# Kernel tuning notes

Measured on AMD Instinct MI355X. Metric: run time of the kernel, lower is better.

Reference implementation:

```python
import jax, jax.numpy as jnp
import numpy as np
from jax import lax

B, N, M = 2, 16384, 4096
C1, C2 = 128, 256
H1, H2 = 256, 128  # mlp = [C1+C2, 256, 128]


def setup_inputs() -> dict:
    key = jax.random.key(0)
    ks = jax.random.split(key, 8)
    return {
        "unknown": jax.random.normal(ks[0], (B, N, 3), jnp.float32),
        "known": jax.random.normal(ks[1], (B, M, 3), jnp.float32),
        "unknow_feats": jax.random.normal(ks[2], (B, C1, N), jnp.float32),
        "known_feats": jax.random.normal(ks[3], (B, C2, M), jnp.float32),
        "W1": jax.random.normal(ks[4], (H1, C1 + C2), jnp.float32) * 0.05,
        "b1": jnp.zeros((H1,), jnp.float32),
        "W2": jax.random.normal(ks[5], (H2, H1), jnp.float32) * 0.05,
        "b2": jnp.zeros((H2,), jnp.float32),
    }


def reference(unknown, known, unknow_feats, known_feats, W1, b1, W2, b2):
    # Pairwise squared distances (B, n, m) via ||a||^2 + ||b||^2 - 2 a.b
    d2 = (
        jnp.sum(unknown * unknown, -1)[:, :, None]
        + jnp.sum(known * known, -1)[:, None, :]
        - 2.0 * jnp.einsum("bnd,bmd->bnm", unknown, known)
    )
    # 3 nearest neighbors
    neg_d2, idx = lax.top_k(-d2, 3)  # (B, n, 3)
    dist = jnp.sqrt(jnp.maximum(-neg_d2, 0.0))  # pointops returns sqrt distances
    dist_recip = 1.0 / (dist + 1e-8)
    weight = dist_recip / jnp.sum(dist_recip, axis=2, keepdims=True)  # (B, n, 3)
    # Gather neighbor features (B, C2, n, 3) and inverse-distance weighted sum
    gathered = jax.vmap(lambda f, i: f[:, i])(known_feats, idx)
    interpolated = jnp.sum(gathered * weight[:, None, :, :], axis=-1)  # (B, C2, n)
    new_features = jnp.concatenate([interpolated, unknow_feats], axis=1)  # (B, C1+C2, n)
    # Shared MLP (1x1 convs, bn=False -> conv bias + ReLU)
    h = jax.nn.relu(jnp.einsum("oc,bcn->bon", W1, new_features) + b1[None, :, None])
    out = jax.nn.relu(jnp.einsum("oc,bcn->bon", W2, h) + b2[None, :, None])
    return out  # (B, mlp[-1], n)
```

## Files before the change

kernel.cpp:

```cpp
#include <hip/hip_runtime.h>
#include <hip/hip_bf16.h>

#define BB 2
#define NN 16384
#define MM 4096
#define C1 128
#define C2 256
#define CIN 384
#define H1 256
#define H2 128
#define PT 32

typedef __attribute__((ext_vector_type(8))) short bf16x8;
typedef __attribute__((ext_vector_type(4))) float f32x4;
typedef __attribute__((ext_vector_type(2))) float f32x2;
typedef __attribute__((ext_vector_type(8))) float f32x8;

__device__ __forceinline__ short f32_to_bf16(float x) {
    unsigned u = __float_as_uint(x);
    u += 0x7fffu + ((u >> 16) & 1u);
    return (short)(u >> 16);
}
__device__ __forceinline__ unsigned pack_bf16x2(float a, float b) {
    __hip_bfloat162 h = __float22bfloat162_rn(make_float2(a, b));
    union { __hip_bfloat162 h; unsigned u; } cv;
    cv.h = h;
    return cv.u;
}

__global__ __launch_bounds__(256) void prep_transpose_kernel(
    const float* __restrict__ KF, float* __restrict__ KT,
    const float* __restrict__ W1, const float* __restrict__ W2,
    const float* __restrict__ known,
    short* __restrict__ W1b, short* __restrict__ W2b,
    float* __restrict__ kpk8)
{
    const int bx = blockIdx.x;
    if (bx < 2048) {
        __shared__ float tl[32][33];
        const int b  = bx >> 10;
        const int c0 = ((bx >> 7) & 7) * 32;
        const int m0 = (bx & 127) * 32;
        const int tx = threadIdx.x & 31;
        const int ty = threadIdx.x >> 5;
        #pragma unroll
        for (int r = 0; r < 4; ++r) {
            int c = ty + r * 8;
            tl[c][tx] = KF[((size_t)b * C2 + c0 + c) * MM + m0 + tx];
        }
        __syncthreads();
        #pragma unroll
        for (int r = 0; r < 4; ++r) {
            int m = ty + r * 8;
            KT[((size_t)b * MM + m0 + m) * C2 + c0 + tx] = tl[tx][m];
        }
    } else {
        int i = (bx - 2048) * 256 + threadIdx.x;
        if (i < H1 * CIN) W1b[i] = f32_to_bf16(W1[i]);
        if (i < H2 * H1)  W2b[i] = f32_to_bf16(W2[i]);
        if (i < BB * MM) {
            float x = known[3 * i + 0], y = known[3 * i + 1], z = known[3 * i + 2];
            float n = fmaf(x, x, fmaf(y, y, z * z));
            int g = i >> 1, j = i & 1;
            float* base = kpk8 + (size_t)g * 8;
            base[0 + j] = x; base[2 + j] = y; base[4 + j] = z; base[6 + j] = n;
        }
    }
}

__global__ __launch_bounds__(1024) void knn3_kernel(
    const float* __restrict__ unknown,
    const float* __restrict__ kpk8,
    int*   __restrict__ idx_out,
    float* __restrict__ w_out)
{
    __shared__ float pdv[16][64][3];
    __shared__ float vf[64];
    __shared__ float msc[64][8];
    __shared__ int   mid[64][8];
    __shared__ int   cnt[64];

    const int b    = blockIdx.y;
    const int tid  = threadIdx.x;
    const int lane = tid & 63;
    const int wv   = __builtin_amdgcn_readfirstlane(tid >> 6);
    const int n    = blockIdx.x * 64 + lane;

    if (tid < 64) cnt[tid] = 0;

    const float ux = unknown[((size_t)b * NN + n) * 3 + 0];
    const float uy = unknown[((size_t)b * NN + n) * 3 + 1];
    const float uz = unknown[((size_t)b * NN + n) * 3 + 2];
    const f32x2 ax2 = {-2.f * ux, -2.f * ux};
    const f32x2 ay2 = {-2.f * uy, -2.f * uy};
    const f32x2 az2 = {-2.f * uz, -2.f * uz};
    const float un = fmaf(ux, ux, fmaf(uy, uy, uz * uz));

    const int gbase = wv * 128;
    const float* __restrict__ kp = kpk8 + ((size_t)b * (MM / 2) + gbase) * 8;

    float v0 = 3e38f, v1 = 3e38f, v2 = 3e38f;
    #pragma unroll 4
    for (int g = 0; g < 128; ++g) {
        const f32x8 G = *(const f32x8*)(kp + (size_t)g * 8);
        const f32x2 kx = __builtin_shufflevector(G, G, 0, 1);
        const f32x2 ky = __builtin_shufflevector(G, G, 2, 3);
        const f32x2 kz = __builtin_shufflevector(G, G, 4, 5);
        const f32x2 kn = __builtin_shufflevector(G, G, 6, 7);
        const f32x2 sc2 = __builtin_elementwise_fma(ax2, kx,
                          __builtin_elementwise_fma(ay2, ky,
                          __builtin_elementwise_fma(az2, kz, kn)));
        float sa = sc2.x;
        v2 = __builtin_amdgcn_fmed3f(v1, sa, v2);
        v1 = __builtin_amdgcn_fmed3f(v0, sa, v1);
        v0 = fminf(sa, v0);
        float sb = sc2.y;
        v2 = __builtin_amdgcn_fmed3f(v1, sb, v2);
        v1 = __builtin_amdgcn_fmed3f(v0, sb, v1);
        v0 = fminf(sb, v0);
    }
    pdv[wv][lane][0] = v0; pdv[wv][lane][1] = v1; pdv[wv][lane][2] = v2;
    __syncthreads();

    if (tid < 64) {
        float r0 = 3e38f, r1 = 3e38f, r2 = 3e38f;
        #pragma unroll
        for (int ww = 0; ww < 16; ++ww) {
            #pragma unroll
            for (int k = 0; k < 3; ++k) {
                float d = pdv[ww][tid][k];
                r2 = __builtin_amdgcn_fmed3f(r1, d, r2);
                r1 = __builtin_amdgcn_fmed3f(r0, d, r1);
                r0 = fminf(d, r0);
            }
        }
        vf[tid] = r2;
    }
    __syncthreads();

    const float v2f = vf[lane];
    #pragma unroll 4
    for (int g = 0; g < 128; ++g) {
        const f32x8 G = *(const f32x8*)(kp + (size_t)g * 8);
        const f32x2 kx = __builtin_shufflevector(G, G, 0, 1);
        const f32x2 ky = __builtin_shufflevector(G, G, 2, 3);
        const f32x2 kz = __builtin_shufflevector(G, G, 4, 5);
        const f32x2 kn = __builtin_shufflevector(G, G, 6, 7);
        const f32x2 sc2 = __builtin_elementwise_fma(ax2, kx,
                          __builtin_elementwise_fma(ay2, ky,
                          __builtin_elementwise_fma(az2, kz, kn)));
        if (fminf(sc2.x, sc2.y) <= v2f) {
            if (sc2.x <= v2f) {
                int c = atomicAdd(&cnt[lane], 1);
                if (c < 8) { msc[lane][c] = sc2.x; mid[lane][c] = (gbase + g) * 2; }
            }
            if (sc2.y <= v2f) {
                int c = atomicAdd(&cnt[lane], 1);
                if (c < 8) { msc[lane][c] = sc2.y; mid[lane][c] = (gbase + g) * 2 + 1; }
            }
        }
    }
    __syncthreads();

    if (tid < 64) {
        const int c = cnt[tid] < 8 ? cnt[tid] : 8;
        float r0 = 3e38f, r1 = 3e38f, r2 = 3e38f;
        int   q0 = 0x7FFFFFFF, q1 = 0x7FFFFFFF, q2 = 0x7FFFFFFF;
        #pragma unroll
        for (int k = 0; k < 8; ++k) {
            float d = (k < c) ? msc[tid][k] : 3e38f;
            int   j = (k < c) ? mid[tid][k] : 0x7FFFFFFF;
            const bool lt0 = (d < r0) || (d == r0 && j < q0);
            const bool lt1 = (d < r1) || (d == r1 && j < q1);
            const bool lt2 = (d < r2) || (d == r2 && j < q2);
            float nr2 = lt1 ? r1 : (lt2 ? d : r2);
            int   nq2 = lt1 ? q1 : (lt2 ? j : q2);
            float nr1 = lt0 ? r0 : (lt1 ? d : r1);
            int   nq1 = lt0 ? q0 : (lt1 ? j : q1);
            float nr0 = lt0 ? d : r0;
            int   nq0 = lt0 ? j : q0;
            r0 = nr0; r1 = nr1; r2 = nr2; q0 = nq0; q1 = nq1; q2 = nq2;
        }
        float d0 = sqrtf(fmaxf(r0 + un, 0.f));
        float d1 = sqrtf(fmaxf(r1 + un, 0.f));
        float d2 = sqrtf(fmaxf(r2 + un, 0.f));
        float i0 = 1.f / (d0 + 1e-8f);
        float i1 = 1.f / (d1 + 1e-8f);
        float i2 = 1.f / (d2 + 1e-8f);
        float s  = i0 + i1 + i2;
        const size_t ob = ((size_t)b * NN + n) * 3;
        idx_out[ob + 0] = q0; idx_out[ob + 1] = q1; idx_out[ob + 2] = q2;
        w_out[ob + 0] = i0 / s; w_out[ob + 1] = i1 / s; w_out[ob + 2] = i2 / s;
    }
}

__global__ __launch_bounds__(256, 3) void fp_mlp_mfma_kernel(
    const float* __restrict__ unknow_feats,
    const float* __restrict__ KT,
    const short* __restrict__ W1b,
    const float* __restrict__ b1,
    const short* __restrict__ W2b,
    const float* __restrict__ b2,
    const int*   __restrict__ idx,
    const float* __restrict__ wgt,
    float* __restrict__ out)
{
    #define XROW 392
    #define HROW 264
    __shared__ short Xs[PT][XROW];
    __shared__ short Hs[PT][HROW];
    __shared__ int   Is[PT * 3];
    __shared__ float Ws[PT * 3];

    const int tid  = threadIdx.x;
    const int blocks_per_b = NN / PT;
    const int b    = blockIdx.x / blocks_per_b;
    const int n0   = (blockIdx.x % blocks_per_b) * PT;
    const int w    = tid >> 6;
    const int lane = tid & 63;
    const int lr   = lane & 15;
    const int lq   = lane >> 4;

    if (tid < PT * 3) {
        const size_t base = ((size_t)b * NN + n0) * 3;
        Is[tid] = idx[base + tid];
        Ws[tid] = wgt[base + tid];
    }
    __syncthreads();

    {
        const float* KTb = KT + (size_t)b * MM * C2;
        const int c4 = (lane << 2);
        #pragma unroll
        for (int pp = 0; pp < PT; pp += 4) {
            const int p = pp + w;
            const int   i0 = Is[3 * p + 0], i1 = Is[3 * p + 1], i2 = Is[3 * p + 2];
            const float w0 = Ws[3 * p + 0], w1 = Ws[3 * p + 1], w2 = Ws[3 * p + 2];
            const float4 A = *(const float4*)(KTb + (size_t)i0 * C2 + c4);
            const float4 Bv = *(const float4*)(KTb + (size_t)i1 * C2 + c4);
            const float4 Cv = *(const float4*)(KTb + (size_t)i2 * C2 + c4);
            float vx = fmaf(w0, A.x, fmaf(w1, Bv.x, w2 * Cv.x));
            float vy = fmaf(w0, A.y, fmaf(w1, Bv.y, w2 * Cv.y));
            float vz = fmaf(w0, A.z, fmaf(w1, Bv.z, w2 * Cv.z));
            float vw = fmaf(w0, A.w, fmaf(w1, Bv.w, w2 * Cv.w));
            uint2 pk;
            pk.x = pack_bf16x2(vx, vy);
            pk.y = pack_bf16x2(vz, vw);
            *(uint2*)&Xs[p][c4] = pk;
        }
        const float* UFb = unknow_feats + (size_t)b * C1 * NN + n0;
        #pragma unroll
        for (int i = 0; i < 4; ++i) {
            int e  = i * 256 + tid;
            int cc = e >> 3;
            int nq = (e & 7) << 2;
            const float4 f = *(const float4*)(UFb + (size_t)cc * NN + nq);
            Xs[nq + 0][C2 + cc] = f32_to_bf16(f.x);
            Xs[nq + 1][C2 + cc] = f32_to_bf16(f.y);
            Xs[nq + 2][C2 + cc] = f32_to_bf16(f.z);
            Xs[nq + 3][C2 + cc] = f32_to_bf16(f.w);
        }
    }
    __syncthreads();

    {
        f32x4 acc[4][2];
        #pragma unroll
        for (int t = 0; t < 4; ++t)
            #pragma unroll
            for (int p = 0; p < 2; ++p) acc[t][p] = (f32x4){0.f, 0.f, 0.f, 0.f};

        #pragma unroll 4
        for (int k0 = 0; k0 < CIN; k0 += 32) {
            bf16x8 a[4], x[2];
            #pragma unroll
            for (int t = 0; t < 4; ++t)
                a[t] = *(const bf16x8*)(W1b + (size_t)(w * 64 + t * 16 + lr) * CIN + k0 + lq * 8);
            #pragma unroll
            for (int p = 0; p < 2; ++p)
                x[p] = *(bf16x8*)&Xs[p * 16 + lr][k0 + lq * 8];
            #pragma unroll
            for (int t = 0; t < 4; ++t)
                #pragma unroll
                for (int p = 0; p < 2; ++p)
                    acc[t][p] = __builtin_amdgcn_mfma_f32_16x16x32_bf16(a[t], x[p], acc[t][p], 0, 0, 0);
        }
        #pragma unroll
        for (int t = 0; t < 4; ++t) {
            const int obase = w * 64 + t * 16 + lq * 4;
            float bb0 = b1[obase + 0], bb1 = b1[obase + 1],
                  bb2 = b1[obase + 2], bb3 = b1[obase + 3];
            #pragma unroll
            for (int p = 0; p < 2; ++p) {
                uint2 pk;
                pk.x = pack_bf16x2(fmaxf(acc[t][p].x + bb0, 0.f),
                                   fmaxf(acc[t][p].y + bb1, 0.f));
                pk.y = pack_bf16x2(fmaxf(acc[t][p].z + bb2, 0.f),
                                   fmaxf(acc[t][p].w + bb3, 0.f));
                *(uint2*)&Hs[p * 16 + lr][obase] = pk;
            }
        }
    }
    __syncthreads();

    {
        f32x4 acc[2][2];
        #pragma unroll
        for (int t = 0; t < 2; ++t)
            #pragma unroll
            for (int p = 0; p < 2; ++p) acc[t][p] = (f32x4){0.f, 0.f, 0.f, 0.f};

        #pragma unroll 4
        for (int k0 = 0; k0 < H1; k0 += 32) {
            bf16x8 a[2], h[2];
            #pragma unroll
            for (int t = 0; t < 2; ++t)
                a[t] = *(const bf16x8*)(W2b + (size_t)(w * 32 + t * 16 + lr) * H1 + k0 + lq * 8);
            #pragma unroll
            for (int p = 0; p < 2; ++p)
                h[p] = *(bf16x8*)&Hs[p * 16 + lr][k0 + lq * 8];
            #pragma unroll
            for (int t = 0; t < 2; ++t)
                #pragma unroll
                for (int p = 0; p < 2; ++p)
                    acc[t][p] = __builtin_amdgcn_mfma_f32_16x16x32_bf16(a[t], h[p], acc[t][p], 0, 0, 0);
        }
        #pragma unroll
        for (int t = 0; t < 2; ++t) {
            const int obase = w * 32 + t * 16 + lq * 4;
            #pragma unroll
            for (int p = 0; p < 2; ++p) {
                const int n = n0 + p * 16 + lr;
                #pragma unroll
                for (int r = 0; r < 4; ++r) {
                    const int o = obase + r;
                    out[((size_t)b * H2 + o) * NN + n] =
                        fmaxf(((const float*)&acc[t][p])[r] + b2[o], 0.f);
                }
            }
        }
    }
    #undef XROW
    #undef HROW
}

extern "C" void kernel_launch(void* const* d_in, const int* in_sizes, int n_in,
                              void* d_out, int out_size, void* d_ws, size_t ws_size,
                              hipStream_t stream) {
    const float* unknown      = (const float*)d_in[0];
    const float* known        = (const float*)d_in[1];
    const float* unknow_feats = (const float*)d_in[2];
    const float* known_feats  = (const float*)d_in[3];
    const float* W1           = (const float*)d_in[4];
    const float* b1           = (const float*)d_in[5];
    const float* W2           = (const float*)d_in[6];
    const float* b2           = (const float*)d_in[7];
    float* out = (float*)d_out;

    char* ws = (char*)d_ws;
    int*    idx  = (int*)(ws);
    float*  wgt  = (float*)(ws + 393216);
    short*  W1b  = (short*)(ws + 786432);
    short*  W2b  = (short*)(ws + 983040);
    float*  kpk8 = (float*)(ws + 1048576);
    float*  KT   = (float*)(ws + 1179648);

    prep_transpose_kernel<<<2048 + 384, 256, 0, stream>>>(
        known_feats, KT, W1, W2, known, W1b, W2b, kpk8);

    dim3 gK(NN / 64, BB);
    knn3_kernel<<<gK, 1024, 0, stream>>>(unknown, kpk8, idx, wgt);

    fp_mlp_mfma_kernel<<<BB * (NN / PT), 256, 0, stream>>>(
        unknow_feats, KT, W1b, b1, W2b, b2, idx, wgt, out);
}
```

Measured before the change: 179.7 us.

## Merge transpose into KNN launch, store gathered features as bf16, share LDS

Splits the known-point packing into its own tiny kernel. The known_feats transpose and the weight conversion now run as extra blocks of the KNN kernel, so they overlap with the neighbor search instead of occupying a separate prep launch. The transposed features are stored as bf16, which halves gather traffic in the MLP kernel, and the gathers are batched into registers before use. The X and H shared-memory tiles are merged into one buffer and launch bounds are raised to 4 blocks per SM to improve occupancy. In exchange, the feature gather adds a bf16 rounding step and register pressure rises from the batched loads.

```diff
diff --git a/kernel.cpp b/kernel.cpp
--- a/kernel.cpp
+++ b/kernel.cpp
@@ -10,6 +10,7 @@
 #define H1 256
 #define H2 128
 #define PT 32
+#define XROW 392
 
 typedef __attribute__((ext_vector_type(8))) short bf16x8;
 typedef __attribute__((ext_vector_type(4))) float f32x4;
@@ -20,6 +21,9 @@
     unsigned u = __float_as_uint(x);
     u += 0x7fffu + ((u >> 16) & 1u);
     return (short)(u >> 16);
+}
+__device__ __forceinline__ float bf16_to_f32(unsigned short u) {
+    union { unsigned u; float f; } c; c.u = ((unsigned)u) << 16; return c.f;
 }
 __device__ __forceinline__ unsigned pack_bf16x2(float a, float b) {
     __hip_bfloat162 h = __float22bfloat162_rn(make_float2(a, b));
@@ -28,175 +32,173 @@
     return cv.u;
 }
 
-__global__ __launch_bounds__(256) void prep_transpose_kernel(
-    const float* __restrict__ KF, float* __restrict__ KT,
-    const float* __restrict__ W1, const float* __restrict__ W2,
-    const float* __restrict__ known,
-    short* __restrict__ W1b, short* __restrict__ W2b,
-    float* __restrict__ kpk8)
+__global__ __launch_bounds__(1024) void kpk_prep_kernel(
+    const float* __restrict__ known, float* __restrict__ kpk8)
 {
-    const int bx = blockIdx.x;
-    if (bx < 2048) {
-        __shared__ float tl[32][33];
-        const int b  = bx >> 10;
-        const int c0 = ((bx >> 7) & 7) * 32;
-        const int m0 = (bx & 127) * 32;
-        const int tx = threadIdx.x & 31;
-        const int ty = threadIdx.x >> 5;
-        #pragma unroll
-        for (int r = 0; r < 4; ++r) {
-            int c = ty + r * 8;
-            tl[c][tx] = KF[((size_t)b * C2 + c0 + c) * MM + m0 + tx];
-        }
-        __syncthreads();
-        #pragma unroll
-        for (int r = 0; r < 4; ++r) {
-            int m = ty + r * 8;
-            KT[((size_t)b * MM + m0 + m) * C2 + c0 + tx] = tl[tx][m];
-        }
-    } else {
-        int i = (bx - 2048) * 256 + threadIdx.x;
-        if (i < H1 * CIN) W1b[i] = f32_to_bf16(W1[i]);
-        if (i < H2 * H1)  W2b[i] = f32_to_bf16(W2[i]);
-        if (i < BB * MM) {
-            float x = known[3 * i + 0], y = known[3 * i + 1], z = known[3 * i + 2];
-            float n = fmaf(x, x, fmaf(y, y, z * z));
-            int g = i >> 1, j = i & 1;
-            float* base = kpk8 + (size_t)g * 8;
-            base[0 + j] = x; base[2 + j] = y; base[4 + j] = z; base[6 + j] = n;
-        }
-    }
-}
-
-__global__ __launch_bounds__(1024) void knn3_kernel(
+    int i = blockIdx.x * 1024 + threadIdx.x;
+    if (i < BB * MM) {
+        float x = known[3 * i + 0], y = known[3 * i + 1], z = known[3 * i + 2];
+        float n = fmaf(x, x, fmaf(y, y, z * z));
+        int g = i >> 1, j = i & 1;
+        float* base = kpk8 + (size_t)g * 8;
+        base[0 + j] = x; base[2 + j] = y; base[4 + j] = z; base[6 + j] = n;
+    }
+}
+
+__global__ __launch_bounds__(1024) void knn_aux_kernel(
     const float* __restrict__ unknown,
     const float* __restrict__ kpk8,
     int*   __restrict__ idx_out,
-    float* __restrict__ w_out)
+    float* __restrict__ w_out,
+    const float* __restrict__ KF,
+    unsigned short* __restrict__ KT16,
+    const float* __restrict__ W1, const float* __restrict__ W2,
+    short* __restrict__ W1b, short* __restrict__ W2b)
 {
     __shared__ float pdv[16][64][3];
     __shared__ float vf[64];
     __shared__ float msc[64][8];
     __shared__ int   mid[64][8];
     __shared__ int   cnt[64];
-
-    const int b    = blockIdx.y;
-    const int tid  = threadIdx.x;
-    const int lane = tid & 63;
-    const int wv   = __builtin_amdgcn_readfirstlane(tid >> 6);
-    const int n    = blockIdx.x * 64 + lane;
-
-    if (tid < 64) cnt[tid] = 0;
-
-    const float ux = unknown[((size_t)b * NN + n) * 3 + 0];
-    const float uy = unknown[((size_t)b * NN + n) * 3 + 1];
-    const float uz = unknown[((size_t)b * NN + n) * 3 + 2];
-    const f32x2 ax2 = {-2.f * ux, -2.f * ux};
-    const f32x2 ay2 = {-2.f * uy, -2.f * uy};
-    const f32x2 az2 = {-2.f * uz, -2.f * uz};
-    const float un = fmaf(ux, ux, fmaf(uy, uy, uz * uz));
-
-    const int gbase = wv * 128;
-    const float* __restrict__ kp = kpk8 + ((size_t)b * (MM / 2) + gbase) * 8;
-
-    float v0 = 3e38f, v1 = 3e38f, v2 = 3e38f;
-    #pragma unroll 4
-    for (int g = 0; g < 128; ++g) {
-        const f32x8 G = *(const f32x8*)(kp + (size_t)g * 8);
-        const f32x2 kx = __builtin_shufflevector(G, G, 0, 1);
-        const f32x2 ky = __builtin_shufflevector(G, G, 2, 3);
-        const f32x2 kz = __builtin_shufflevector(G, G, 4, 5);
-        const f32x2 kn = __builtin_shufflevector(G, G, 6, 7);
-        const f32x2 sc2 = __builtin_elementwise_fma(ax2, kx,
-                          __builtin_elementwise_fma(ay2, ky,
-                          __builtin_elementwise_fma(az2, kz, kn)));
-        float sa = sc2.x;
-        v2 = __builtin_amdgcn_fmed3f(v1, sa, v2);
-        v1 = __builtin_amdgcn_fmed3f(v0, sa, v1);
-        v0 = fminf(sa, v0);
-        float sb = sc2.y;
-        v2 = __builtin_amdgcn_fmed3f(v1, sb, v2);
-        v1 = __builtin_amdgcn_fmed3f(v0, sb, v1);
-        v0 = fminf(sb, v0);
-    }
-    pdv[wv][lane][0] = v0; pdv[wv][lane][1] = v1; pdv[wv][lane][2] = v2;
-    __syncthreads();
-
-    if (tid < 64) {
-        float r0 = 3e38f, r1 = 3e38f, r2 = 3e38f;
-        #pragma unroll
-        for (int ww = 0; ww < 16; ++ww) {
-            #pragma unroll
-            for (int k = 0; k < 3; ++k) {
-                float d = pdv[ww][tid][k];
-                r2 = __builtin_amdgcn_fmed3f(r1, d, r2);
-                r1 = __builtin_amdgcn_fmed3f(r0, d, r1);
-                r0 = fminf(d, r0);
+    __shared__ float tl[32][33];
+
+    const int bx  = blockIdx.x;
+    const int tid = threadIdx.x;
+
+    if (bx < 512) {
+        const int lane = tid & 63;
+        const int wv   = __builtin_amdgcn_readfirstlane(tid >> 6);
+        const int b    = bx >> 8;
+        const int n    = (bx & 255) * 64 + lane;
+
+        if (tid < 64) cnt[tid] = 0;
+
+        const float ux = unknown[((size_t)b * NN + n) * 3 + 0];
+        const float uy = unknown[((size_t)b * NN + n) * 3 + 1];
+        const float uz = unknown[((size_t)b * NN + n) * 3 + 2];
+        const f32x2 ax2 = {-2.f * ux, -2.f * ux};
+        const f32x2 ay2 = {-2.f * uy, -2.f * uy};
+        const f32x2 az2 = {-2.f * uz, -2.f * uz};
+        const float un = fmaf(ux, ux, fmaf(uy, uy, uz * uz));
+
+        const int gbase = wv * 128;
+        const float* __restrict__ kp = kpk8 + ((size_t)b * (MM / 2) + gbase) * 8;
+
+        float v0 = 3e38f, v1 = 3e38f, v2 = 3e38f;
+        #pragma unroll 4
+        for (int g = 0; g < 128; ++g) {
+            const f32x8 G = *(const f32x8*)(kp + (size_t)g * 8);
+            const f32x2 kx = __builtin_shufflevector(G, G, 0, 1);
+            const f32x2 ky = __builtin_shufflevector(G, G, 2, 3);
+            const f32x2 kz = __builtin_shufflevector(G, G, 4, 5);
+            const f32x2 kn = __builtin_shufflevector(G, G, 6, 7);
+            const f32x2 sc2 = __builtin_elementwise_fma(ax2, kx,
+                              __builtin_elementwise_fma(ay2, ky,
+                              __builtin_elementwise_fma(az2, kz, kn)));
+            float sa = sc2.x;
+            v2 = __builtin_amdgcn_fmed3f(v1, sa, v2);
+            v1 = __builtin_amdgcn_fmed3f(v0, sa, v1);
+            v0 = fminf(sa, v0);
+            float sb = sc2.y;
+            v2 = __builtin_amdgcn_fmed3f(v1, sb, v2);
+            v1 = __builtin_amdgcn_fmed3f(v0, sb, v1);
+            v0 = fminf(sb, v0);
+        }
+        pdv[wv][lane][0] = v0; pdv[wv][lane][1] = v1; pdv[wv][lane][2] = v2;
+        __syncthreads();
+
+        if (tid < 64) {
+            float r0 = 3e38f, r1 = 3e38f, r2 = 3e38f;
+            #pragma unroll
+            for (int ww = 0; ww < 16; ++ww) {
+                #pragma unroll
+                for (int k = 0; k < 3; ++k) {
+                    float d = pdv[ww][tid][k];
+                    r2 = __builtin_amdgcn_fmed3f(r1, d, r2);
+                    r1 = __builtin_amdgcn_fmed3f(r0, d, r1);
+                    r0 = fminf(d, r0);
+                }
             }
-        }
-        vf[tid] = r2;
-    }
-    __syncthreads();
-
-    const float v2f = vf[lane];
-    #pragma unroll 4
-    for (int g = 0; g < 128; ++g) {
-        const f32x8 G = *(const f32x8*)(kp + (size_t)g * 8);
-        const f32x2 kx = __builtin_shufflevector(G, G, 0, 1);
-        const f32x2 ky = __builtin_shufflevector(G, G, 2, 3);
-        const f32x2 kz = __builtin_shufflevector(G, G, 4, 5);
-        const f32x2 kn = __builtin_shufflevector(G, G, 6, 7);
-        const f32x2 sc2 = __builtin_elementwise_fma(ax2, kx,
-                          __builtin_elementwise_fma(ay2, ky,
-                          __builtin_elementwise_fma(az2, kz, kn)));
-        if (fminf(sc2.x, sc2.y) <= v2f) {
-            if (sc2.x <= v2f) {
-                int c = atomicAdd(&cnt[lane], 1);
-                if (c < 8) { msc[lane][c] = sc2.x; mid[lane][c] = (gbase + g) * 2; }
+            vf[tid] = r2;
+        }
+        __syncthreads();
+
+        const float v2f = vf[lane];
+        #pragma unroll 4
+        for (int g = 0; g < 128; ++g) {
+            const f32x8 G = *(const f32x8*)(kp + (size_t)g * 8);
+            const f32x2 kx = __builtin_shufflevector(G, G, 0, 1);
+            const f32x2 ky = __builtin_shufflevector(G, G, 2, 3);
+            const f32x2 kz = __builtin_shufflevector(G, G, 4, 5);
+            const f32x2 kn = __builtin_shufflevector(G, G, 6, 7);
+            const f32x2 sc2 = __builtin_elementwise_fma(ax2, kx,
+                              __builtin_elementwise_fma(ay2, ky,
+                              __builtin_elementwise_fma(az2, kz, kn)));
+            if (fminf(sc2.x, sc2.y) <= v2f) {
+                if (sc2.x <= v2f) {
+                    int c = atomicAdd(&cnt[lane], 1);
+                    if (c < 8) { msc[lane][c] = sc2.x; mid[lane][c] = (gbase + g) * 2; }
+                }
+                if (sc2.y <= v2f) {
+                    int c = atomicAdd(&cnt[lane], 1);
+                    if (c < 8) { msc[lane][c] = sc2.y; mid[lane][c] = (gbase + g) * 2 + 1; }
+                }
             }
-            if (sc2.y <= v2f) {
-                int c = atomicAdd(&cnt[lane], 1);
-                if (c < 8) { msc[lane][c] = sc2.y; mid[lane][c] = (gbase + g) * 2 + 1; }
+        }
+        __syncthreads();
+
+        if (tid < 64) {
+            const int c = cnt[tid] < 8 ? cnt[tid] : 8;
+            float r0 = 3e38f, r1 = 3e38f, r2 = 3e38f;
+            int   q0 = 0x7FFFFFFF, q1 = 0x7FFFFFFF, q2 = 0x7FFFFFFF;
+            #pragma unroll
+            for (int k = 0; k < 8; ++k) {
+                float d = (k < c) ? msc[tid][k] : 3e38f;
+                int   j = (k < c) ? mid[tid][k] : 0x7FFFFFFF;
+                const bool lt0 = (d < r0) || (d == r0 && j < q0);
+                const bool lt1 = (d < r1) || (d == r1 && j < q1);
+                const bool lt2 = (d < r2) || (d == r2 && j < q2);
+                float nr2 = lt1 ? r1 : (lt2 ? d : r2);
+                int   nq2 = lt1 ? q1 : (lt2 ? j : q2);
+                float nr1 = lt0 ? r0 : (lt1 ? d : r1);
+                int   nq1 = lt0 ? q0 : (lt1 ? j : q1);
+                float nr0 = lt0 ? d : r0;
+                int   nq0 = lt0 ? j : q0;
+                r0 = nr0; r1 = nr1; r2 = nr2; q0 = nq0; q1 = nq1; q2 = nq2;
             }
-        }
-    }
-    __syncthreads();
-
-    if (tid < 64) {
-        const int c = cnt[tid] < 8 ? cnt[tid] : 8;
-        float r0 = 3e38f, r1 = 3e38f, r2 = 3e38f;
-        int   q0 = 0x7FFFFFFF, q1 = 0x7FFFFFFF, q2 = 0x7FFFFFFF;
-        #pragma unroll
-        for (int k = 0; k < 8; ++k) {
-            float d = (k < c) ? msc[tid][k] : 3e38f;
-            int   j = (k < c) ? mid[tid][k] : 0x7FFFFFFF;
-            const bool lt0 = (d < r0) || (d == r0 && j < q0);
-            const bool lt1 = (d < r1) || (d == r1 && j < q1);
-            const bool lt2 = (d < r2) || (d == r2 && j < q2);
-            float nr2 = lt1 ? r1 : (lt2 ? d : r2);
-            int   nq2 = lt1 ? q1 : (lt2 ? j : q2);
-            float nr1 = lt0 ? r0 : (lt1 ? d : r1);
-            int   nq1 = lt0 ? q0 : (lt1 ? j : q1);
-            float nr0 = lt0 ? d : r0;
-            int   nq0 = lt0 ? j : q0;
-            r0 = nr0; r1 = nr1; r2 = nr2; q0 = nq0; q1 = nq1; q2 = nq2;
-        }
-        float d0 = sqrtf(fmaxf(r0 + un, 0.f));
-        float d1 = sqrtf(fmaxf(r1 + un, 0.f));
-        float d2 = sqrtf(fmaxf(r2 + un, 0.f));
-        float i0 = 1.f / (d0 + 1e-8f);
-        float i1 = 1.f / (d1 + 1e-8f);
-        float i2 = 1.f / (d2 + 1e-8f);
-        float s  = i0 + i1 + i2;
-        const size_t ob = ((size_t)b * NN + n) * 3;
-        idx_out[ob + 0] = q0; idx_out[ob + 1] = q1; idx_out[ob + 2] = q2;
-        w_out[ob + 0] = i0 / s; w_out[ob + 1] = i1 / s; w_out[ob + 2] = i2 / s;
-    }
-}
-
-__global__ __launch_bounds__(256, 3) void fp_mlp_mfma_kernel(
+            float d0 = sqrtf(fmaxf(r0 + un, 0.f));
+            float d1 = sqrtf(fmaxf(r1 + un, 0.f));
+            float d2 = sqrtf(fmaxf(r2 + un, 0.f));
+            float i0 = 1.f / (d0 + 1e-8f);
+            float i1 = 1.f / (d1 + 1e-8f);
+            float i2 = 1.f / (d2 + 1e-8f);
+            float s  = i0 + i1 + i2;
+            const size_t ob = ((size_t)(bx >> 8) * NN + n) * 3;
+            idx_out[ob + 0] = q0; idx_out[ob + 1] = q1; idx_out[ob + 2] = q2;
+            w_out[ob + 0] = i0 / s; w_out[ob + 1] = i1 / s; w_out[ob + 2] = i2 / s;
+        }
+    } else if (bx < 2560) {
+        const int t  = bx - 512;
+        const int b  = t >> 10;
+        const int c0 = ((t >> 7) & 7) * 32;
+        const int m0 = (t & 127) * 32;
+        if (tid < 1024) {
+            const int tx = tid & 31;
+            const int ty = tid >> 5;
+            tl[ty][tx] = KF[((size_t)b * C2 + c0 + ty) * MM + m0 + tx];
+            __syncthreads();
+            KT16[((size_t)b * MM + m0 + ty) * C2 + c0 + tx] = (unsigned short)f32_to_bf16(tl[tx][ty]);
+        }
+    } else {
+        int i = (bx - 2560) * 1024 + tid;
+        if (i < H1 * CIN) W1b[i] = f32_to_bf16(W1[i]);
+        if (i < H2 * H1)  W2b[i] = f32_to_bf16(W2[i]);
+    }
+}
+
+__global__ __launch_bounds__(256, 4) void fp_mlp_mfma_kernel(
     const float* __restrict__ unknow_feats,
-    const float* __restrict__ KT,
+    const unsigned short* __restrict__ KT16,
     const short* __restrict__ W1b,
     const float* __restrict__ b1,
     const short* __restrict__ W2b,
@@ -205,10 +207,7 @@
     const float* __restrict__ wgt,
     float* __restrict__ out)
 {
-    #define XROW 392
-    #define HROW 264
-    __shared__ short Xs[PT][XROW];
-    __shared__ short Hs[PT][HROW];
+    __shared__ short XH[PT][XROW];
     __shared__ int   Is[PT * 3];
     __shared__ float Ws[PT * 3];
 
@@ -229,24 +228,28 @@
     __syncthreads();
 
     {
-        const float* KTb = KT + (size_t)b * MM * C2;
+        const unsigned short* KTb = KT16 + (size_t)b * MM * C2;
         const int c4 = (lane << 2);
-        #pragma unroll
-        for (int pp = 0; pp < PT; pp += 4) {
-            const int p = pp + w;
-            const int   i0 = Is[3 * p + 0], i1 = Is[3 * p + 1], i2 = Is[3 * p + 2];
+        ushort4 g[8][3];
+        #pragma unroll
+        for (int i = 0; i < 8; ++i) {
+            const int p = i * 4 + w;
+            g[i][0] = *(const ushort4*)(KTb + (size_t)Is[3 * p + 0] * C2 + c4);
+            g[i][1] = *(const ushort4*)(KTb + (size_t)Is[3 * p + 1] * C2 + c4);
+            g[i][2] = *(const ushort4*)(KTb + (size_t)Is[3 * p + 2] * C2 + c4);
+        }
+        #pragma unroll
+        for (int i = 0; i < 8; ++i) {
+            const int p = i * 4 + w;
             const float w0 = Ws[3 * p + 0], w1 = Ws[3 * p + 1], w2 = Ws[3 * p + 2];
-            const float4 A = *(const float4*)(KTb + (size_t)i0 * C2 + c4);
-            const float4 Bv = *(const float4*)(KTb + (size_t)i1 * C2 + c4);
-            const float4 Cv = *(const float4*)(KTb + (size_t)i2 * C2 + c4);
-            float vx = fmaf(w0, A.x, fmaf(w1, Bv.x, w2 * Cv.x));
-            float vy = fmaf(w0, A.y, fmaf(w1, Bv.y, w2 * Cv.y));
-            float vz = fmaf(w0, A.z, fmaf(w1, Bv.z, w2 * Cv.z));
-            float vw = fmaf(w0, A.w, fmaf(w1, Bv.w, w2 * Cv.w));
+            float vx = fmaf(w0, bf16_to_f32(g[i][0].x), fmaf(w1, bf16_to_f32(g[i][1].x), w2 * bf16_to_f32(g[i][2].x)));
+            float vy = fmaf(w0, bf16_to_f32(g[i][0].y), fmaf(w1, bf16_to_f32(g[i][1].y), w2 * bf16_to_f32(g[i][2].y)));
+            float vz = fmaf(w0, bf16_to_f32(g[i][0].z), fmaf(w1, bf16_to_f32(g[i][1].z), w2 * bf16_to_f32(g[i][2].z)));
+            float vw = fmaf(w0, bf16_to_f32(g[i][0].w), fmaf(w1, bf16_to_f32(g[i][1].w), w2 * bf16_to_f32(g[i][2].w)));
             uint2 pk;
             pk.x = pack_bf16x2(vx, vy);
             pk.y = pack_bf16x2(vz, vw);
-            *(uint2*)&Xs[p][c4] = pk;
+            *(uint2*)&XH[p][c4] = pk;
         }
         const float* UFb = unknow_feats + (size_t)b * C1 * NN + n0;
         #pragma unroll
@@ -255,60 +258,60 @@
             int cc = e >> 3;
             int nq = (e & 7) << 2;
             const float4 f = *(const float4*)(UFb + (size_t)cc * NN + nq);
-            Xs[nq + 0][C2 + cc] = f32_to_bf16(f.x);
-            Xs[nq + 1][C2 + cc] = f32_to_bf16(f.y);
-            Xs[nq + 2][C2 + cc] = f32_to_bf16(f.z);
-            Xs[nq + 3][C2 + cc] = f32_to_bf16(f.w);
+            XH[nq + 0][C2 + cc] = f32_to_bf16(f.x);
+            XH[nq + 1][C2 + cc] = f32_to_bf16(f.y);
+            XH[nq + 2][C2 + cc] = f32_to_bf16(f.z);
+            XH[nq + 3][C2 + cc] = f32_to_bf16(f.w);
         }
     }
     __syncthreads();
 
+    f32x4 acc[4][2];
+    #pragma unroll
+    for (int t = 0; t < 4; ++t)
+        #pragma unroll
+        for (int p = 0; p < 2; ++p) acc[t][p] = (f32x4){0.f, 0.f, 0.f, 0.f};
+
+    #pragma unroll 4
+    for (int k0 = 0; k0 < CIN; k0 += 32) {
+        bf16x8 a[4], x[2];
+        #pragma unroll
+        for (int t = 0; t < 4; ++t)
+            a[t] = *(const bf16x8*)(W1b + (size_t)(w * 64 + t * 16 + lr) * CIN + k0 + lq * 8);
+        #pragma unroll
+        for (int p = 0; p < 2; ++p)
+            x[p] = *(bf16x8*)&XH[p * 16 + lr][k0 + lq * 8];
+        #pragma unroll
+        for (int t = 0; t < 4; ++t)
+            #pragma unroll
+            for (int p = 0; p < 2; ++p)
+                acc[t][p] = __builtin_amdgcn_mfma_f32_16x16x32_bf16(a[t], x[p], acc[t][p], 0, 0, 0);
+    }
+    __syncthreads();
+
+    #pragma unroll
+    for (int t = 0; t < 4; ++t) {
+        const int obase = w * 64 + t * 16 + lq * 4;
+        float bb0 = b1[obase + 0], bb1 = b1[obase + 1],
+              bb2 = b1[obase + 2], bb3 = b1[obase + 3];
+        #pragma unroll
+        for (int p = 0; p < 2; ++p) {
+            uint2 pk;
+            pk.x = pack_bf16x2(fmaxf(acc[t][p].x + bb0, 0.f),
+                               fmaxf(acc[t][p].y + bb1, 0.f));
+            pk.y = pack_bf16x2(fmaxf(acc[t][p].z + bb2, 0.f),
+                               fmaxf(acc[t][p].w + bb3, 0.f));
+            *(uint2*)&XH[p * 16 + lr][obase] = pk;
+        }
+    }
+    __syncthreads();
+
     {
-        f32x4 acc[4][2];
-        #pragma unroll
-        for (int t = 0; t < 4; ++t)
-            #pragma unroll
-            for (int p = 0; p < 2; ++p) acc[t][p] = (f32x4){0.f, 0.f, 0.f, 0.f};
-
-        #pragma unroll 4
-        for (int k0 = 0; k0 < CIN; k0 += 32) {
-            bf16x8 a[4], x[2];
-            #pragma unroll
-            for (int t = 0; t < 4; ++t)
-                a[t] = *(const bf16x8*)(W1b + (size_t)(w * 64 + t * 16 + lr) * CIN + k0 + lq * 8);
-            #pragma unroll
-            for (int p = 0; p < 2; ++p)
-                x[p] = *(bf16x8*)&Xs[p * 16 + lr][k0 + lq * 8];
-            #pragma unroll
-            for (int t = 0; t < 4; ++t)
-                #pragma unroll
-                for (int p = 0; p < 2; ++p)
-                    acc[t][p] = __builtin_amdgcn_mfma_f32_16x16x32_bf16(a[t], x[p], acc[t][p], 0, 0, 0);
-        }
-        #pragma unroll
-        for (int t = 0; t < 4; ++t) {
-            const int obase = w * 64 + t * 16 + lq * 4;
-            float bb0 = b1[obase + 0], bb1 = b1[obase + 1],
-                  bb2 = b1[obase + 2], bb3 = b1[obase + 3];
-            #pragma unroll
-            for (int p = 0; p < 2; ++p) {
-                uint2 pk;
-                pk.x = pack_bf16x2(fmaxf(acc[t][p].x + bb0, 0.f),
-                                   fmaxf(acc[t][p].y + bb1, 0.f));
-                pk.y = pack_bf16x2(fmaxf(acc[t][p].z + bb2, 0.f),
-                                   fmaxf(acc[t][p].w + bb3, 0.f));
-                *(uint2*)&Hs[p * 16 + lr][obase] = pk;
-            }
-        }
-    }
-    __syncthreads();
-
-    {
-        f32x4 acc[2][2];
+        f32x4 acc2[2][2];
         #pragma unroll
         for (int t = 0; t < 2; ++t)
             #pragma unroll
-            for (int p = 0; p < 2; ++p) acc[t][p] = (f32x4){0.f, 0.f, 0.f, 0.f};
+            for (int p = 0; p < 2; ++p) acc2[t][p] = (f32x4){0.f, 0.f, 0.f, 0.f};
 
         #pragma unroll 4
         for (int k0 = 0; k0 < H1; k0 += 32) {
@@ -318,12 +321,12 @@
                 a[t] = *(const bf16x8*)(W2b + (size_t)(w * 32 + t * 16 + lr) * H1 + k0 + lq * 8);
             #pragma unroll
             for (int p = 0; p < 2; ++p)
-                h[p] = *(bf16x8*)&Hs[p * 16 + lr][k0 + lq * 8];
+                h[p] = *(bf16x8*)&XH[p * 16 + lr][k0 + lq * 8];
             #pragma unroll
             for (int t = 0; t < 2; ++t)
                 #pragma unroll
                 for (int p = 0; p < 2; ++p)
-                    acc[t][p] = __builtin_amdgcn_mfma_f32_16x16x32_bf16(a[t], h[p], acc[t][p], 0, 0, 0);
+                    acc2[t][p] = __builtin_amdgcn_mfma_f32_16x16x32_bf16(a[t], h[p], acc2[t][p], 0, 0, 0);
         }
         #pragma unroll
         for (int t = 0; t < 2; ++t) {
@@ -335,13 +338,11 @@
                 for (int r = 0; r < 4; ++r) {
                     const int o = obase + r;
                     out[((size_t)b * H2 + o) * NN + n] =
-                        fmaxf(((const float*)&acc[t][p])[r] + b2[o], 0.f);
+                        fmaxf(((const float*)&acc2[t][p])[r] + b2[o], 0.f);
                 }
             }
         }
     }
-    #undef XROW
-    #undef HROW
 }
 
 extern "C" void kernel_launch(void* const* d_in, const int* in_sizes, int n_in,
@@ -358,19 +359,18 @@
     float* out = (float*)d_out;
 
     char* ws = (char*)d_ws;
-    int*    idx  = (int*)(ws);
-    float*  wgt  = (float*)(ws + 393216);
-    short*  W1b  = (short*)(ws + 786432);
-    short*  W2b  = (short*)(ws + 983040);
-    float*  kpk8 = (float*)(ws + 1048576);
-    float*  KT   = (float*)(ws + 1179648);
-
-    prep_transpose_kernel<<<2048 + 384, 256, 0, stream>>>(
-        known_feats, KT, W1, W2, known, W1b, W2b, kpk8);
-
-    dim3 gK(NN / 64, BB);
-    knn3_kernel<<<gK, 1024, 0, stream>>>(unknown, kpk8, idx, wgt);
+    int*            idx  = (int*)(ws);
+    float*          wgt  = (float*)(ws + 393216);
+    short*          W1b  = (short*)(ws + 786432);
+    short*          W2b  = (short*)(ws + 983040);
+    float*          kpk8 = (float*)(ws + 1048576);
+    unsigned short* KT16 = (unsigned short*)(ws + 1179648);
+
+    kpk_prep_kernel<<<8, 1024, 0, stream>>>(known, kpk8);
+
+    knn_aux_kernel<<<2656, 1024, 0, stream>>>(
+        unknown, kpk8, idx, wgt, known_feats, KT16, W1, W2, W1b, W2b);
 
     fp_mlp_mfma_kernel<<<BB * (NN / PT), 256, 0, stream>>>(
-        unknow_feats, KT, W1b, b1, W2b, b2, idx, wgt, out);
-}
+        unknow_feats, KT16, W1b, b1, W2b, b2, idx, wgt, out);
+}
```

Result: faster. 166.2 us (-7.5%).
